# Performance work log

Measured on AMD Instinct MI355X. Metric: run time of the kernel, lower is better.

Reference implementation:

```python
import jax, jax.numpy as jnp
import numpy as np

TAU = 2.0          # LIF membrane time constant (decay_input=True)
V_TH = 1.0         # spike threshold, hard reset to 0
SG_ALPHA = 2.0     # ATan surrogate gradient alpha

@jax.custom_vjp
def spike(x):
    # Heaviside spike with ATan surrogate gradient
    return (x >= 0).astype(x.dtype)

def _spike_fwd(x):
    return spike(x), x

def _spike_bwd(x, g):
    sg = (SG_ALPHA / 2.0) / (1.0 + (jnp.pi / 2.0 * SG_ALPHA * x) ** 2)
    return (g * sg,)

spike.defvjp(_spike_fwd, _spike_bwd)

def setup_inputs() -> dict:
    key = jax.random.key(0)
    ks = jax.random.split(key, 12)
    B, T, D_IN, H, D_OUT = 256, 250, 700, 128, 20
    def lin(k, fan_in, fan_out):
        bound = 1.0 / np.sqrt(fan_in)
        kw, kb = jax.random.split(k)
        W = jax.random.uniform(kw, (fan_in, fan_out), jnp.float32, -bound, bound)
        b = jax.random.uniform(kb, (fan_out,), jnp.float32, -bound, bound)
        return W, b
    W1, b1 = lin(ks[0], D_IN, H)
    rcW1, rcb1 = lin(ks[1], H, H)
    W2, b2 = lin(ks[2], H, H)
    rcW2, rcb2 = lin(ks[3], H, H)
    W3, b3 = lin(ks[4], H, D_OUT)
    x = jax.random.normal(ks[5], (B, T, D_IN), jnp.float32)
    return {"x": x, "W1": W1, "b1": b1, "rcW1": rcW1, "rcb1": rcb1,
            "W2": W2, "b2": b2, "rcW2": rcW2, "rcb2": rcb2,
            "W3": W3, "b3": b3}

def _lif(v, u):
    # decay_input LIF: v += (u - v)/tau ; spike ; hard reset to 0
    v = v + (u - v) / TAU
    s = spike(v - V_TH)
    v = v * (1.0 - s)
    return v, s

def reference(x, W1, b1, rcW1, rcb1, W2, b2, rcW2, rcb2, W3, b3):
    B = x.shape[0]
    H = W1.shape[1]
    xt = jnp.swapaxes(x, 0, 1)  # [T, B, D_in] — matches permute(1,0,2)

    def step(carry, x_t):
        y1, v1, y2, v2, acc = carry
        h1 = x_t @ W1 + b1                      # first Linear
        u1 = y1 @ rcW1 + rcb1 + h1              # recurrent container 1
        v1, y1 = _lif(v1, u1)
        h2 = y1 @ W2 + b2                       # mid Linear
        u2 = y2 @ rcW2 + rcb2 + h2              # recurrent container 2
        v2, y2 = _lif(v2, u2)
        out_t = y2 @ W3 + b3                    # readout
        return (y1, v1, y2, v2, acc + out_t), None

    z = jnp.zeros((B, H), x.dtype)
    acc0 = jnp.zeros((B, W3.shape[1]), x.dtype)
    (y1, v1, y2, v2, acc), _ = jax.lax.scan(step, (z, z, z, z, acc0), xt)
    return acc  # res.sum(0): [B, out_dim]
```

## Files before the change

### kernel.cpp

```cpp
#include <hip/hip_runtime.h>
#include <cstdint>
#include <cstddef>

#define Bb   256
#define Tt   250
#define DIN  700
#define Hh   128
#define DOUT 20

constexpr int BM  = 128;
constexpr int BK  = 20;
constexpr int BN  = 128;
constexpr int BMP = BM + 4;

__device__ __forceinline__ int bswz(int g) { return g ^ (g >> 3); }

__global__ __launch_bounds__(256, 2) void gemm_h1(const float* __restrict__ x,
                                                  const float* __restrict__ W1,
                                                  const float* __restrict__ b1,
                                                  float* __restrict__ H1) {
    __shared__ float Ast[BK][BMP];
    __shared__ float Bs[BK][BN];

    const int tid = threadIdx.x;
    const int tx  = tid & 15;
    const int ty  = tid >> 4;
    const int m0  = blockIdx.x * BM;

    const int c0 = bswz(tx * 2) * 4;
    const int c1 = bswz(tx * 2 + 1) * 4;

    float acc[8][8];
#pragma unroll
    for (int r = 0; r < 8; ++r)
#pragma unroll
        for (int c = 0; c < 8; ++c) acc[r][c] = 0.f;

    for (int k0 = 0; k0 < DIN; k0 += BK) {
#pragma unroll
        for (int idx = tid; idx < 640; idx += 256) {
            int row = idx / 5;
            int kq  = (idx - row * 5) * 4;
            const float4 v =
                *(const float4*)&x[(size_t)(m0 + row) * DIN + (k0 + kq)];
            Ast[kq + 0][row] = v.x;
            Ast[kq + 1][row] = v.y;
            Ast[kq + 2][row] = v.z;
            Ast[kq + 3][row] = v.w;
        }
#pragma unroll
        for (int idx = tid; idx < 640; idx += 256) {
            int kr = idx >> 5;
            int g  = idx & 31;
            *(float4*)&Bs[kr][bswz(g) * 4] =
                *(const float4*)&W1[(size_t)(k0 + kr) * BN + g * 4];
        }
        __syncthreads();

#pragma unroll
        for (int kk = 0; kk < BK; ++kk) {
            float a[8], bv[8];
            *(float4*)&a[0]  = *(const float4*)&Ast[kk][ty * 8];
            *(float4*)&a[4]  = *(const float4*)&Ast[kk][ty * 8 + 4];
            *(float4*)&bv[0] = *(const float4*)&Bs[kk][c0];
            *(float4*)&bv[4] = *(const float4*)&Bs[kk][c1];
#pragma unroll
            for (int r = 0; r < 8; ++r)
#pragma unroll
                for (int c = 0; c < 8; ++c)
                    acc[r][c] = fmaf(a[r], bv[c], acc[r][c]);
        }
        __syncthreads();
    }

    float bb[8];
#pragma unroll
    for (int c = 0; c < 8; ++c) bb[c] = b1[tx * 8 + c];

#pragma unroll
    for (int r = 0; r < 8; ++r) {
        size_t row = (size_t)(m0 + ty * 8 + r);
        float4 o0, o1;
        o0.x = acc[r][0] + bb[0]; o0.y = acc[r][1] + bb[1];
        o0.z = acc[r][2] + bb[2]; o0.w = acc[r][3] + bb[3];
        o1.x = acc[r][4] + bb[4]; o1.y = acc[r][5] + bb[5];
        o1.z = acc[r][6] + bb[6]; o1.w = acc[r][7] + bb[7];
        *(float4*)&H1[row * Hh + tx * 8]     = o0;
        *(float4*)&H1[row * Hh + tx * 8 + 4] = o1;
    }
}

__global__ __launch_bounds__(64) void recurrent(
    const float* __restrict__ H1,   const float* __restrict__ rcW1,
    const float* __restrict__ rcb1, const float* __restrict__ W2,
    const float* __restrict__ b2,   const float* __restrict__ rcW2,
    const float* __restrict__ rcb2, const float* __restrict__ W3,
    const float* __restrict__ b3,   float* __restrict__ out) {

    __shared__ float scnt[Hh];

    const int lane = threadIdx.x;
    const int b    = blockIdx.x;

    const float rcb1x = rcb1[lane], rcb1y = rcb1[lane + 64];
    const float bb2x  = b2[lane]      + rcb2[lane];
    const float bb2y  = b2[lane + 64] + rcb2[lane + 64];
    const float* __restrict__ h1p = H1 + (size_t)b * Tt * Hh;

    float v1x = 0.f, v1y = 0.f, v2x = 0.f, v2y = 0.f;
    float cntx = 0.f, cnty = 0.f;
    float u1gx = 0.f, u1gy = 0.f;
    float u2gx = 0.f, u2gy = 0.f;

    float h1xs[4], h1ys[4];
#pragma unroll
    for (int j = 0; j < 4; ++j) {
        h1xs[j] = h1p[j * Hh + lane];
        h1ys[j] = h1p[j * Hh + lane + 64];
    }

#define STEP(T, J)                                                            \
    {                                                                         \
        const int t_ = (T);                                                   \
                \
        const float u1xv = h1xs[J] + rcb1x + u1gx;                            \
        const float u1yv = h1ys[J] + rcb1y + u1gy;                            \
        int tp = t_ + 4; tp = (tp < Tt) ? tp : (Tt - 1);                      \
        h1xs[J] = h1p[(size_t)tp * Hh + lane];                                \
        h1ys[J] = h1p[(size_t)tp * Hh + lane + 64];                           \
        v1x = v1x + (u1xv - v1x) * 0.5f;                                      \
        v1y = v1y + (u1yv - v1y) * 0.5f;                                      \
        const bool s1x = (v1x >= 1.0f);                                       \
        const bool s1y = (v1y >= 1.0f);                                       \
        if (s1x) v1x = 0.f;                                                   \
        if (s1y) v1y = 0.f;                                                   \
        const unsigned long long a0 = __ballot((int)s1x);                     \
        const unsigned long long a1 = __ballot((int)s1y);                     \
            \
        float uW2x = 0.f, uW2y = 0.f, g1x = 0.f, g1y = 0.f;                   \
        if (a0 | a1) {                                                        \
            unsigned long long m = a0;                                        \
            int base = 0;                                                     \
            for (int hlf = 0; hlf < 2; ++hlf) {                               \
                while (m) {                                                   \
                    const int k = (int)__ffsll(m) - 1 + base;                 \
                    m &= (m - 1ull);                                          \
                    const float* __restrict__ pw = W2 + k * Hh;               \
                    const float* __restrict__ pr = rcW1 + k * Hh;             \
                    uW2x += pw[lane]; uW2y += pw[lane + 64];                  \
                    g1x  += pr[lane]; g1y  += pr[lane + 64];                  \
                }                                                             \
                m = a1; base = 64;                                            \
            }                                                                 \
        }                                                                     \
        u1gx = g1x; u1gy = g1y;                                               \
                                                         \
        const float u2xv = bb2x + uW2x + u2gx;                                \
        const float u2yv = bb2y + uW2y + u2gy;                                \
        v2x = v2x + (u2xv - v2x) * 0.5f;                                      \
        v2y = v2y + (u2yv - v2y) * 0.5f;                                      \
        const bool s2x = (v2x >= 1.0f);                                       \
        const bool s2y = (v2y >= 1.0f);                                       \
        if (s2x) v2x = 0.f;                                                   \
        if (s2y) v2y = 0.f;                                                   \
        cntx += s2x ? 1.f : 0.f;                                              \
        cnty += s2y ? 1.f : 0.f;                                              \
        const unsigned long long c0m = __ballot((int)s2x);                    \
        const unsigned long long c1m = __ballot((int)s2y);                    \
        float g2x = 0.f, g2y = 0.f;                                           \
        if (c0m | c1m) {                                                      \
            unsigned long long m = c0m;                                       \
            int base = 0;                                                     \
            for (int hlf = 0; hlf < 2; ++hlf) {                               \
                while (m) {                                                   \
                    const int k = (int)__ffsll(m) - 1 + base;                 \
                    m &= (m - 1ull);                                          \
                    const float* __restrict__ pr = rcW2 + k * Hh;             \
                    g2x += pr[lane]; g2y += pr[lane + 64];                    \
                }                                                             \
                m = c1m; base = 64;                                           \
            }                                                                 \
        }                                                                     \
        u2gx = g2x; u2gy = g2y;                                               \
    }

    for (int tb = 0; tb < 62; ++tb) {
        const int t0 = tb * 4;
        STEP(t0 + 0, 0)
        STEP(t0 + 1, 1)
        STEP(t0 + 2, 2)
        STEP(t0 + 3, 3)
    }
    STEP(248, 0)
    STEP(249, 1)
#undef STEP

    scnt[lane]      = cntx;
    scnt[lane + 64] = cnty;
    __syncthreads();
    if (lane < DOUT) {
        float o = (float)Tt * b3[lane];
#pragma unroll 8
        for (int k = 0; k < Hh; ++k) o += scnt[k] * W3[k * DOUT + lane];
        out[b * DOUT + lane] = o;
    }
}

extern "C" void kernel_launch(void* const* d_in, const int* in_sizes, int n_in,
                              void* d_out, int out_size, void* d_ws, size_t ws_size,
                              hipStream_t stream) {
    const float* x    = (const float*)d_in[0];
    const float* W1   = (const float*)d_in[1];
    const float* b1   = (const float*)d_in[2];
    const float* rcW1 = (const float*)d_in[3];
    const float* rcb1 = (const float*)d_in[4];
    const float* W2   = (const float*)d_in[5];
    const float* b2   = (const float*)d_in[6];
    const float* rcW2 = (const float*)d_in[7];
    const float* rcb2 = (const float*)d_in[8];
    const float* W3   = (const float*)d_in[9];
    const float* b3   = (const float*)d_in[10];

    float* out = (float*)d_out;
    float* H1  = (float*)d_ws;

    gemm_h1<<<(Bb * Tt) / BM, 256, 0, stream>>>(x, W1, b1, H1);
    recurrent<<<Bb, 64, 0, stream>>>(H1, rcW1, rcb1, W2, b2, rcW2, rcb2, W3,
                                     b3, out);
}
```

Before: 447.8 us.

## Stream H1 into an LDS ring via async global_load_lds and prefetch GEMM tiles

The recurrent kernel now streams each batch row's H1 sequence into a 64KB LDS ring buffer in 16KB chunks, using asynchronous global-to-LDS loads and explicit vmcnt waits. Per-step H1 reads therefore come from LDS instead of global memory, which takes global load latency off the serial timestep chain. The GEMM kernel also gains register double-buffering, prefetching the next K tile from global memory while the current tile is being computed. The costs are much higher LDS use per block, which may limit occupancy, and fragile hand-counted waitcnt logic.

```diff
diff --git a/kernel.cpp b/kernel.cpp
--- a/kernel.cpp
+++ b/kernel.cpp
@@ -30,32 +30,58 @@
     const int c0 = bswz(tx * 2) * 4;
     const int c1 = bswz(tx * 2 + 1) * 4;
 
+    const int arow0 = tid / 5,         akq0 = (tid - arow0 * 5) * 4;
+    const int ai1   = tid + 256;
+    const int arow1 = ai1 / 5,         akq1 = (ai1 - arow1 * 5) * 4;
+    const int ai2   = tid + 512;
+    const int arow2 = ai2 / 5,         akq2 = (ai2 - arow2 * 5) * 4;
+    const int bkr0  = tid >> 5,        bg   = tid & 31;
+    const int bcs   = bswz(bg) * 4;
+    const bool has2 = (tid < 128);
+
+    float4 va0, va1, va2, vb0, vb1, vb2;
+
+#define LOAD_TILE(K0)                                                         \
+    {                                                                         \
+        const int k0_ = (K0);                                                 \
+        va0 = *(const float4*)&x[(size_t)(m0 + arow0) * DIN + (k0_ + akq0)];  \
+        va1 = *(const float4*)&x[(size_t)(m0 + arow1) * DIN + (k0_ + akq1)];  \
+        if (has2)                                                             \
+            va2 = *(const float4*)&x[(size_t)(m0 + arow2) * DIN + (k0_ + akq2)]; \
+        vb0 = *(const float4*)&W1[(size_t)(k0_ + bkr0) * BN + bg * 4];        \
+        vb1 = *(const float4*)&W1[(size_t)(k0_ + bkr0 + 8) * BN + bg * 4];    \
+        if (has2)                                                             \
+            vb2 = *(const float4*)&W1[(size_t)(k0_ + bkr0 + 16) * BN + bg * 4]; \
+    }
+
+#define STORE_TILE()                                                          \
+    {                                                                         \
+        Ast[akq0 + 0][arow0] = va0.x; Ast[akq0 + 1][arow0] = va0.y;           \
+        Ast[akq0 + 2][arow0] = va0.z; Ast[akq0 + 3][arow0] = va0.w;           \
+        Ast[akq1 + 0][arow1] = va1.x; Ast[akq1 + 1][arow1] = va1.y;           \
+        Ast[akq1 + 2][arow1] = va1.z; Ast[akq1 + 3][arow1] = va1.w;           \
+        if (has2) {                                                           \
+            Ast[akq2 + 0][arow2] = va2.x; Ast[akq2 + 1][arow2] = va2.y;       \
+            Ast[akq2 + 2][arow2] = va2.z; Ast[akq2 + 3][arow2] = va2.w;       \
+        }                                                                     \
+        *(float4*)&Bs[bkr0][bcs]      = vb0;                                  \
+        *(float4*)&Bs[bkr0 + 8][bcs]  = vb1;                                  \
+        if (has2) *(float4*)&Bs[bkr0 + 16][bcs] = vb2;                        \
+    }
+
     float acc[8][8];
 #pragma unroll
     for (int r = 0; r < 8; ++r)
 #pragma unroll
         for (int c = 0; c < 8; ++c) acc[r][c] = 0.f;
 
+    LOAD_TILE(0);
+    STORE_TILE();
+    __syncthreads();
+
     for (int k0 = 0; k0 < DIN; k0 += BK) {
-#pragma unroll
-        for (int idx = tid; idx < 640; idx += 256) {
-            int row = idx / 5;
-            int kq  = (idx - row * 5) * 4;
-            const float4 v =
-                *(const float4*)&x[(size_t)(m0 + row) * DIN + (k0 + kq)];
-            Ast[kq + 0][row] = v.x;
-            Ast[kq + 1][row] = v.y;
-            Ast[kq + 2][row] = v.z;
-            Ast[kq + 3][row] = v.w;
-        }
-#pragma unroll
-        for (int idx = tid; idx < 640; idx += 256) {
-            int kr = idx >> 5;
-            int g  = idx & 31;
-            *(float4*)&Bs[kr][bswz(g) * 4] =
-                *(const float4*)&W1[(size_t)(k0 + kr) * BN + g * 4];
-        }
-        __syncthreads();
+        const bool more = (k0 + BK < DIN);
+        if (more) LOAD_TILE(k0 + BK);
 
 #pragma unroll
         for (int kk = 0; kk < BK; ++kk) {
@@ -71,7 +97,11 @@
                     acc[r][c] = fmaf(a[r], bv[c], acc[r][c]);
         }
         __syncthreads();
-    }
+        if (more) STORE_TILE();
+        __syncthreads();
+    }
+#undef LOAD_TILE
+#undef STORE_TILE
 
     float bb[8];
 #pragma unroll
@@ -90,6 +120,24 @@
     }
 }
 
+
+#define WAITV(N)                                                       \
+    asm volatile("s_waitcnt vmcnt(" #N ")" ::: "memory");              \
+    __builtin_amdgcn_sched_barrier(0)
+
+__device__ __forceinline__ void issue_chunk(const float* __restrict__ h1p,
+                                            float* ring, int c, int n,
+                                            int lane) {
+    const char* g = (const char*)h1p + (size_t)c * 16384 + (size_t)lane * 16;
+    char* l = (char*)ring + ((c & 3) * 16384);
+    for (int i = 0; i < n; ++i) {
+        __builtin_amdgcn_global_load_lds(
+            (const __attribute__((address_space(1))) uint32_t*)(g + (size_t)i * 1024),
+            (__attribute__((address_space(3))) uint32_t*)(l + i * 1024),
+            16, 0, 0);
+    }
+}
+
 __global__ __launch_bounds__(64) void recurrent(
     const float* __restrict__ H1,   const float* __restrict__ rcW1,
     const float* __restrict__ rcb1, const float* __restrict__ W2,
@@ -97,7 +145,7 @@
     const float* __restrict__ rcb2, const float* __restrict__ W3,
     const float* __restrict__ b3,   float* __restrict__ out) {
 
-    __shared__ float scnt[Hh];
+    __shared__ float ring[128 * Hh];
 
     const int lane = threadIdx.x;
     const int b    = blockIdx.x;
@@ -112,22 +160,28 @@
     float u1gx = 0.f, u1gy = 0.f;
     float u2gx = 0.f, u2gy = 0.f;
 
+    issue_chunk(h1p, ring, 0, 16, lane);
+    issue_chunk(h1p, ring, 1, 16, lane);
+    issue_chunk(h1p, ring, 2, 16, lane);
+    WAITV(32);
+
     float h1xs[4], h1ys[4];
 #pragma unroll
     for (int j = 0; j < 4; ++j) {
-        h1xs[j] = h1p[j * Hh + lane];
-        h1ys[j] = h1p[j * Hh + lane + 64];
+        h1xs[j] = ring[(j << 7) + lane];
+        h1ys[j] = ring[(j << 7) + lane + 64];
     }
 
 #define STEP(T, J)                                                            \
     {                                                                         \
         const int t_ = (T);                                                   \
-                \
+            \
         const float u1xv = h1xs[J] + rcb1x + u1gx;                            \
         const float u1yv = h1ys[J] + rcb1y + u1gy;                            \
         int tp = t_ + 4; tp = (tp < Tt) ? tp : (Tt - 1);                      \
-        h1xs[J] = h1p[(size_t)tp * Hh + lane];                                \
-        h1ys[J] = h1p[(size_t)tp * Hh + lane + 64];                           \
+        const float* rp_ = &ring[(tp & 127) << 7];                            \
+        h1xs[J] = rp_[lane];                                                  \
+        h1ys[J] = rp_[lane + 64];                                             \
         v1x = v1x + (u1xv - v1x) * 0.5f;                                      \
         v1y = v1y + (u1yv - v1y) * 0.5f;                                      \
         const bool s1x = (v1x >= 1.0f);                                       \
@@ -184,24 +238,34 @@
         u2gx = g2x; u2gy = g2y;                                               \
     }
 
-    for (int tb = 0; tb < 62; ++tb) {
-        const int t0 = tb * 4;
-        STEP(t0 + 0, 0)
-        STEP(t0 + 1, 1)
-        STEP(t0 + 2, 2)
-        STEP(t0 + 3, 3)
+#pragma unroll 1
+    for (int c = 0; c < 8; ++c) {
+        if (c <= 4) issue_chunk(h1p, ring, c + 3, (c == 4) ? 13 : 16, lane);
+        if (c < 5)       { WAITV(16); }
+        else if (c == 5) { WAITV(13); }
+        else             { WAITV(0);  }
+        const int ng = (c < 7) ? 8 : 6;
+        const int t0 = c << 5;
+#pragma unroll 1
+        for (int g = 0; g < ng; ++g) {
+            const int t = t0 + (g << 2);
+            STEP(t + 0, 0)
+            STEP(t + 1, 1)
+            STEP(t + 2, 2)
+            STEP(t + 3, 3)
+        }
     }
     STEP(248, 0)
     STEP(249, 1)
 #undef STEP
 
-    scnt[lane]      = cntx;
-    scnt[lane + 64] = cnty;
+    ring[lane]      = cntx;
+    ring[lane + 64] = cnty;
     __syncthreads();
     if (lane < DOUT) {
         float o = (float)Tt * b3[lane];
 #pragma unroll 8
-        for (int k = 0; k < Hh; ++k) o += scnt[k] * W3[k * DOUT + lane];
+        for (int k = 0; k < Hh; ++k) o += ring[k] * W3[k * DOUT + lane];
         out[b * DOUT + lane] = o;
     }
 }
```

After: 1.495 ms. 234% more time.

## Stage recurrent weights in LDS and prefetch H1 via async LDS ring

Applied to the files above, without the earlier changes.

The recurrent kernel now copies W2 and rcW1 into LDS (128KB total) with global_load_lds, so the spike-driven row gathers read LDS instead of global memory. It also streams per-batch H1 through a 32-step LDS ring buffer filled asynchronously with explicit vmcnt waits. The sparse gathers are batched four rows at a time to expose memory-level parallelism, and the rcW2 gather for layer 2 is deferred and loaded one step ahead so its latency overlaps the next step. The large LDS footprint limits occupancy to one 64-thread block per CU and adds upfront copy latency per block.

```diff
diff --git a/kernel.cpp b/kernel.cpp
--- a/kernel.cpp
+++ b/kernel.cpp
@@ -90,6 +90,31 @@
     }
 }
 
+
+#define WAITV(N)                                                       \
+    asm volatile("s_waitcnt vmcnt(" #N ")" ::: "memory");              \
+    __builtin_amdgcn_sched_barrier(0)
+
+__device__ __forceinline__ void gll16(const void* g, void* l) {
+    __builtin_amdgcn_global_load_lds(
+        (const __attribute__((address_space(1))) uint32_t*)g,
+        (__attribute__((address_space(3))) uint32_t*)l, 16, 0, 0);
+}
+
+__device__ __forceinline__ void issue_chunk(const char* hg, char* ringb,
+                                            int c, int n) {
+    const char* g = hg + (size_t)c * 4096;
+    char* l = ringb + (c & 3) * 4096;
+    for (int i = 0; i < n; ++i) gll16(g + (size_t)i * 1024, l + i * 1024);
+}
+
+#define EXTR(K)                                                        \
+    if (mlo) { K = (int)__ffsll(mlo) - 1; mlo &= mlo - 1ull; }         \
+    else     { K = 64 + (int)__ffsll(mhi) - 1; mhi &= mhi - 1ull; }
+#define EXTR2(K)                                                       \
+    if (mlo)      { K = (int)__ffsll(mlo) - 1; mlo &= mlo - 1ull; }    \
+    else if (mhi) { K = 64 + (int)__ffsll(mhi) - 1; mhi &= mhi - 1ull; }
+
 __global__ __launch_bounds__(64) void recurrent(
     const float* __restrict__ H1,   const float* __restrict__ rcW1,
     const float* __restrict__ rcb1, const float* __restrict__ W2,
@@ -97,7 +122,9 @@
     const float* __restrict__ rcb2, const float* __restrict__ W3,
     const float* __restrict__ b3,   float* __restrict__ out) {
 
-    __shared__ float scnt[Hh];
+    __shared__ float W2ls[Hh * Hh];
+    __shared__ float rcW1ls[Hh * Hh];
+    __shared__ float ring[32 * Hh];
 
     const int lane = threadIdx.x;
     const int b    = blockIdx.x;
@@ -107,27 +134,46 @@
     const float bb2y  = b2[lane + 64] + rcb2[lane + 64];
     const float* __restrict__ h1p = H1 + (size_t)b * Tt * Hh;
 
+    {
+        const char* g2 = (const char*)W2 + lane * 16;
+        const char* g1 = (const char*)rcW1 + lane * 16;
+        char* l2 = (char*)W2ls;
+        char* l1 = (char*)rcW1ls;
+#pragma unroll 1
+        for (int i = 0; i < 64; ++i) gll16(g2 + (size_t)i * 1024, l2 + i * 1024);
+#pragma unroll 1
+        for (int i = 0; i < 64; ++i) gll16(g1 + (size_t)i * 1024, l1 + i * 1024);
+    }
+    const char* hg = (const char*)h1p + lane * 16;
+    char* ringb = (char*)ring;
+    issue_chunk(hg, ringb, 0, 4);
+    issue_chunk(hg, ringb, 1, 4);
+    issue_chunk(hg, ringb, 2, 4);
+    WAITV(4);
+
     float v1x = 0.f, v1y = 0.f, v2x = 0.f, v2y = 0.f;
     float cntx = 0.f, cnty = 0.f;
     float u1gx = 0.f, u1gy = 0.f;
-    float u2gx = 0.f, u2gy = 0.f;
+    float l0x = 0.f, l0y = 0.f, l1x = 0.f, l1y = 0.f, l2x = 0.f, l2y = 0.f;
+    bool  f0 = false, f1 = false, f2 = false;
 
     float h1xs[4], h1ys[4];
 #pragma unroll
     for (int j = 0; j < 4; ++j) {
-        h1xs[j] = h1p[j * Hh + lane];
-        h1ys[j] = h1p[j * Hh + lane + 64];
+        h1xs[j] = ring[(j << 7) + lane];
+        h1ys[j] = ring[(j << 7) + lane + 64];
     }
 
 #define STEP(T, J)                                                            \
     {                                                                         \
         const int t_ = (T);                                                   \
-                \
+           \
         const float u1xv = h1xs[J] + rcb1x + u1gx;                            \
         const float u1yv = h1ys[J] + rcb1y + u1gy;                            \
         int tp = t_ + 4; tp = (tp < Tt) ? tp : (Tt - 1);                      \
-        h1xs[J] = h1p[(size_t)tp * Hh + lane];                                \
-        h1ys[J] = h1p[(size_t)tp * Hh + lane + 64];                           \
+        const float* rp_ = &ring[(tp & 31) << 7];                             \
+        h1xs[J] = rp_[lane];                                                  \
+        h1ys[J] = rp_[lane + 64];                                             \
         v1x = v1x + (u1xv - v1x) * 0.5f;                                      \
         v1y = v1y + (u1yv - v1y) * 0.5f;                                      \
         const bool s1x = (v1x >= 1.0f);                                       \
@@ -136,25 +182,37 @@
         if (s1y) v1y = 0.f;                                                   \
         const unsigned long long a0 = __ballot((int)s1x);                     \
         const unsigned long long a1 = __ballot((int)s1y);                     \
-            \
+          \
         float uW2x = 0.f, uW2y = 0.f, g1x = 0.f, g1y = 0.f;                   \
         if (a0 | a1) {                                                        \
-            unsigned long long m = a0;                                        \
-            int base = 0;                                                     \
-            for (int hlf = 0; hlf < 2; ++hlf) {                               \
-                while (m) {                                                   \
-                    const int k = (int)__ffsll(m) - 1 + base;                 \
-                    m &= (m - 1ull);                                          \
-                    const float* __restrict__ pw = W2 + k * Hh;               \
-                    const float* __restrict__ pr = rcW1 + k * Hh;             \
-                    uW2x += pw[lane]; uW2y += pw[lane + 64];                  \
-                    g1x  += pr[lane]; g1y  += pr[lane + 64];                  \
-                }                                                             \
-                m = a1; base = 64;                                            \
+            unsigned long long mlo = a0, mhi = a1;                            \
+            while (mlo | mhi) {                                               \
+                int k0; int k1 = -1; int k2 = -1; int k3 = -1;                \
+                EXTR(k0) EXTR2(k1) EXTR2(k2) EXTR2(k3)                        \
+                const int i0 = k0 << 7;                                       \
+                const int i1 = (k1 >= 0 ? k1 : k0) << 7;                      \
+                const int i2 = (k2 >= 0 ? k2 : k0) << 7;                      \
+                const int i3 = (k3 >= 0 ? k3 : k0) << 7;                      \
+                const float w0x = W2ls[i0 + lane],   w0y = W2ls[i0 + 64 + lane];   \
+                const float r0x = rcW1ls[i0 + lane], r0y = rcW1ls[i0 + 64 + lane]; \
+                const float w1x = W2ls[i1 + lane],   w1y = W2ls[i1 + 64 + lane];   \
+                const float r1x = rcW1ls[i1 + lane], r1y = rcW1ls[i1 + 64 + lane]; \
+                const float w2x = W2ls[i2 + lane],   w2y = W2ls[i2 + 64 + lane];   \
+                const float r2x = rcW1ls[i2 + lane], r2y = rcW1ls[i2 + 64 + lane]; \
+                const float w3x = W2ls[i3 + lane],   w3y = W2ls[i3 + 64 + lane];   \
+                const float r3x = rcW1ls[i3 + lane], r3y = rcW1ls[i3 + 64 + lane]; \
+                uW2x += w0x; uW2y += w0y; g1x += r0x; g1y += r0y;             \
+                if (k1 >= 0) { uW2x += w1x; uW2y += w1y; g1x += r1x; g1y += r1y; } \
+                if (k2 >= 0) { uW2x += w2x; uW2y += w2y; g1x += r2x; g1y += r2y; } \
+                if (k3 >= 0) { uW2x += w3x; uW2y += w3y; g1x += r3x; g1y += r3y; } \
             }                                                                 \
         }                                                                     \
         u1gx = g1x; u1gy = g1y;                                               \
-                                                         \
+              \
+        const float u2gx =                                                    \
+            ((f0 ? l0x : 0.f) + (f1 ? l1x : 0.f)) + (f2 ? l2x : 0.f);         \
+        const float u2gy =                                                    \
+            ((f0 ? l0y : 0.f) + (f1 ? l1y : 0.f)) + (f2 ? l2y : 0.f);         \
         const float u2xv = bb2x + uW2x + u2gx;                                \
         const float u2yv = bb2y + uW2y + u2gy;                                \
         v2x = v2x + (u2xv - v2x) * 0.5f;                                      \
@@ -167,41 +225,62 @@
         cnty += s2y ? 1.f : 0.f;                                              \
         const unsigned long long c0m = __ballot((int)s2x);                    \
         const unsigned long long c1m = __ballot((int)s2y);                    \
-        float g2x = 0.f, g2y = 0.f;                                           \
+               \
+        f0 = false; f1 = false; f2 = false;                                   \
         if (c0m | c1m) {                                                      \
-            unsigned long long m = c0m;                                       \
-            int base = 0;                                                     \
-            for (int hlf = 0; hlf < 2; ++hlf) {                               \
-                while (m) {                                                   \
-                    const int k = (int)__ffsll(m) - 1 + base;                 \
-                    m &= (m - 1ull);                                          \
-                    const float* __restrict__ pr = rcW2 + k * Hh;             \
-                    g2x += pr[lane]; g2y += pr[lane + 64];                    \
+            unsigned long long mlo = c0m, mhi = c1m;                          \
+            const int n2 = __popcll(c0m) + __popcll(c1m);                     \
+            if (n2 <= 3) {                                                    \
+                int k0; int k1 = -1; int k2 = -1;                             \
+                EXTR(k0) EXTR2(k1) EXTR2(k2)                                  \
+                const float* p0 = rcW2 + ((size_t)k0 << 7);                   \
+                const float* p1 = rcW2 + ((size_t)(k1 >= 0 ? k1 : k0) << 7);  \
+                const float* p2 = rcW2 + ((size_t)(k2 >= 0 ? k2 : k0) << 7);  \
+                l0x = p0[lane]; l0y = p0[lane + 64];                          \
+                l1x = p1[lane]; l1y = p1[lane + 64];                          \
+                l2x = p2[lane]; l2y = p2[lane + 64];                          \
+                f0 = true; f1 = (k1 >= 0); f2 = (k2 >= 0);                    \
+            } else {                        \
+                float sx = 0.f, sy = 0.f;                                     \
+                while (mlo | mhi) {                                           \
+                    int kk; EXTR(kk)                                          \
+                    const float* pr = rcW2 + ((size_t)kk << 7);               \
+                    sx += pr[lane]; sy += pr[lane + 64];                      \
                 }                                                             \
-                m = c1m; base = 64;                                           \
+                l0x = sx; l0y = sy;                                           \
+                l1x = 0.f; l1y = 0.f; l2x = 0.f; l2y = 0.f;                   \
+                f0 = true;                                                    \
             }                                                                 \
         }                                                                     \
-        u2gx = g2x; u2gy = g2y;                                               \
-    }
-
-    for (int tb = 0; tb < 62; ++tb) {
-        const int t0 = tb * 4;
-        STEP(t0 + 0, 0)
-        STEP(t0 + 1, 1)
-        STEP(t0 + 2, 2)
-        STEP(t0 + 3, 3)
-    }
+    }
+
+#pragma unroll 1
+    for (int c = 0; c < 31; ++c) {
+        if (c <= 27)      issue_chunk(hg, ringb, c + 3, 4);
+        else if (c == 28) issue_chunk(hg, ringb, 31, 1);
+        if (c <= 27) { WAITV(8); } else { WAITV(0); }
+        const int t0 = c << 3;
+#pragma unroll 1
+        for (int g = 0; g < 2; ++g) {
+            const int t = t0 + (g << 2);
+            STEP(t + 0, 0)
+            STEP(t + 1, 1)
+            STEP(t + 2, 2)
+            STEP(t + 3, 3)
+        }
+    }
+    WAITV(0);
     STEP(248, 0)
     STEP(249, 1)
 #undef STEP
 
-    scnt[lane]      = cntx;
-    scnt[lane + 64] = cnty;
+    ring[lane]      = cntx;
+    ring[lane + 64] = cnty;
     __syncthreads();
     if (lane < DOUT) {
         float o = (float)Tt * b3[lane];
 #pragma unroll 8
-        for (int k = 0; k < Hh; ++k) o += scnt[k] * W3[k * DOUT + lane];
+        for (int k = 0; k < Hh; ++k) o += ring[k] * W3[k * DOUT + lane];
         out[b * DOUT + lane] = o;
     }
 }
```

New measurement: 460.8 us. 2.9% more time.
